# Kernel tuning notes

Measured on AMD Instinct MI355X. Metric: run time of the kernel, lower is better.

The kernel has to match this reference:

```python
import jax, jax.numpy as jnp
import numpy as np

B, L, LIP = 1, 2048, 64
HID, H, D = 3072, 24, 128
MLP = 4 * HID
CTX = 4096
EPS = 1e-6


def setup_inputs() -> dict:
    key = jax.random.key(0)
    ks = jax.random.split(key, 10)
    rn = lambda k, shape, s=1.0: jax.random.normal(k, shape, jnp.float32) * s
    x = rn(ks[0], (B, L, HID))
    vec = rn(ks[1], (B, HID))
    image_proj = rn(ks[2], (B, LIP, CTX))
    # Flux-style RoPE table: [1, 1, L, D//2, 2, 2] rotation matrices
    pos = jnp.arange(L, dtype=jnp.float32)[:, None]
    inv_freq = 1.0 / (10000.0 ** (jnp.arange(0, D, 2, dtype=jnp.float32) / D))
    ang = pos * inv_freq[None, :]                      # [L, D//2]
    cos, sin = jnp.cos(ang), jnp.sin(ang)
    pe = jnp.stack([jnp.stack([cos, -sin], -1), jnp.stack([sin, cos], -1)], -2)
    pe = pe[None, None].astype(jnp.float32)            # [1,1,L,D//2,2,2]
    return dict(
        x=x, vec=vec, pe=pe, image_proj=image_proj, ip_scale=jnp.float32(1.0),
        mod_lin_w=rn(ks[3], (3 * HID, HID), 0.02), mod_lin_b=jnp.zeros((3 * HID,), jnp.float32),
        linear1_w=rn(ks[4], (3 * HID + MLP, HID), 0.02), linear1_b=jnp.zeros((3 * HID + MLP,), jnp.float32),
        linear2_w=rn(ks[5], (HID, HID + MLP), 0.02), linear2_b=jnp.zeros((HID,), jnp.float32),
        q_norm_scale=jnp.ones((D,), jnp.float32), k_norm_scale=jnp.ones((D,), jnp.float32),
        ip_k_w=rn(ks[6], (HID, CTX), 0.02), ip_v_w=rn(ks[7], (HID, CTX), 0.02),
    )


def _layernorm(x):
    mu = jnp.mean(x, -1, keepdims=True)
    var = jnp.mean(jnp.square(x - mu), -1, keepdims=True)
    return (x - mu) * jax.lax.rsqrt(var + EPS)


def _rmsnorm(x, scale):
    return x * jax.lax.rsqrt(jnp.mean(jnp.square(x), -1, keepdims=True) + EPS) * scale


def _apply_rope(xq, pe):
    b, h, l, d = xq.shape
    xq_ = xq.reshape(b, h, l, d // 2, 1, 2)
    out = pe[..., 0] * xq_[..., 0] + pe[..., 1] * xq_[..., 1]  # [b,h,l,d//2,2]
    return out.reshape(b, h, l, d)


def _sdpa(q, k, v):
    scale = 1.0 / np.sqrt(q.shape[-1])
    s = jnp.einsum('bhqd,bhkd->bhqk', q, k) * scale
    return jnp.einsum('bhqk,bhkd->bhqd', jax.nn.softmax(s, axis=-1), v)


def _forward(x, vec, pe, image_proj, ip_scale, mod_lin_w, mod_lin_b,
             linear1_w, linear1_b, linear2_w, linear2_b,
             q_norm_scale, k_norm_scale, ip_k_w, ip_v_w):
    # modulation: shift, scale, gate from silu(vec)
    mod = jax.nn.silu(vec) @ mod_lin_w.T + mod_lin_b   # [B, 3*HID]
    shift, scale, gate = [m[:, None, :] for m in jnp.split(mod, 3, axis=-1)]
    x_mod = (1.0 + scale) * _layernorm(x) + shift
    h = x_mod @ linear1_w.T + linear1_b                # [B, L, 3*HID + MLP]
    qkv, mlp = h[..., :3 * HID], h[..., 3 * HID:]
    qkv = qkv.reshape(B, L, 3, H, D).transpose(2, 0, 3, 1, 4)  # [3,B,H,L,D]
    q, k, v = qkv[0], qkv[1], qkv[2]
    q = _rmsnorm(q, q_norm_scale)
    k = _rmsnorm(k, k_norm_scale)
    # main attention with RoPE
    attn1 = _sdpa(_apply_rope(q, pe), _apply_rope(k, pe), v)   # [B,H,L,D]
    attn1 = attn1.transpose(0, 2, 1, 3).reshape(B, L, HID)
    # IP-adapter cross-attention (query = q after QK-norm, no RoPE)
    ip_k = (image_proj @ ip_k_w.T).reshape(B, LIP, H, D).transpose(0, 2, 1, 3)
    ip_v = (image_proj @ ip_v_w.T).reshape(B, LIP, H, D).transpose(0, 2, 1, 3)
    ip_attn = _sdpa(q, ip_k, ip_v).transpose(0, 2, 1, 3).reshape(B, L, HID)
    attn_out = attn1 + ip_scale * ip_attn
    fused = jnp.concatenate([attn_out, jax.nn.gelu(mlp, approximate=True)], axis=-1)
    output = fused @ linear2_w.T + linear2_b
    return x + gate * output


def reference(x, vec, pe, image_proj, ip_scale, mod_lin_w, mod_lin_b,
              linear1_w, linear1_b, linear2_w, linear2_b,
              q_norm_scale, k_norm_scale, ip_k_w, ip_v_w):
    return _forward(x, vec, pe, image_proj, ip_scale, mod_lin_w, mod_lin_b,
                    linear1_w, linear1_b, linear2_w, linear2_b,
                    q_norm_scale, k_norm_scale, ip_k_w, ip_v_w)
```

## Files before the change

### kernel.cpp

```cpp
#include <hip/hip_runtime.h>
#include <hip/hip_bf16.h>
#include <math.h>

typedef __bf16 bf16_t;
typedef __bf16 bf16x8 __attribute__((ext_vector_type(8)));
typedef __bf16 bf16x4 __attribute__((ext_vector_type(4)));
typedef __bf16 bf16x2 __attribute__((ext_vector_type(2)));
typedef float  f32x4  __attribute__((ext_vector_type(4)));

#define HIDN 3072
#define LQ   2048
#define NH   24
#define HD   128
#define N1   21504
#define N2   15360
#define KIP  4096

__device__ __forceinline__ f32x4 mfma16(bf16x8 a, bf16x8 b, f32x4 c) {
    return __builtin_amdgcn_mfma_f32_16x16x32_bf16(a, b, c, 0, 0, 0);
}

__device__ __forceinline__ float wave_sum64(float v) {
#pragma unroll
    for (int off = 1; off < 64; off <<= 1) v += __shfl_xor(v, off);
    return v;
}

__global__ void k_convert(const float* __restrict__ in, bf16_t* __restrict__ out, int n4) {
    int i = blockIdx.x * blockDim.x + threadIdx.x;
    if (i < n4) {
        float4 f = ((const float4*)in)[i];
        bf16x4 h = {(bf16_t)f.x, (bf16_t)f.y, (bf16_t)f.z, (bf16_t)f.w};
        *(bf16x4*)(out + (size_t)i * 4) = h;
    }
}

__global__ __launch_bounds__(256) void k_mod_gemv(const float* __restrict__ vec,
                                                  const float* __restrict__ W,
                                                  const float* __restrict__ b,
                                                  float* __restrict__ mod) {
    int row  = blockIdx.x * 4 + (threadIdx.x >> 6);
    int lane = threadIdx.x & 63;
    const float4* W4 = (const float4*)(W + (size_t)row * HIDN);
    const float4* V4 = (const float4*)vec;
    float s = 0.f;
#pragma unroll
    for (int i = 0; i < 12; i++) {
        float4 w = W4[lane + i * 64];
        float4 v = V4[lane + i * 64];
        s += w.x * (v.x / (1.f + __expf(-v.x)));
        s += w.y * (v.y / (1.f + __expf(-v.y)));
        s += w.z * (v.z / (1.f + __expf(-v.z)));
        s += w.w * (v.w / (1.f + __expf(-v.w)));
    }
    s = wave_sum64(s);
    if (lane == 0) mod[row] = s + b[row];
}

__global__ __launch_bounds__(256) void k_ln_mod(const float* __restrict__ x,
                                                const float* __restrict__ mod,
                                                bf16_t* __restrict__ x_mod) {
    int row = blockIdx.x, tid = threadIdx.x;
    const float* xr = x + (size_t)row * HIDN;
    float v[12];
    float s = 0.f, ss = 0.f;
#pragma unroll
    for (int p = 0; p < 12; p++) {
        v[p] = xr[tid + p * 256];
        s += v[p]; ss += v[p] * v[p];
    }
    s = wave_sum64(s); ss = wave_sum64(ss);
    __shared__ float red[8];
    int wave = tid >> 6, lane = tid & 63;
    if (lane == 0) { red[wave] = s; red[4 + wave] = ss; }
    __syncthreads();
    float S  = red[0] + red[1] + red[2] + red[3];
    float SS = red[4] + red[5] + red[6] + red[7];
    float mean = S * (1.f / HIDN);
    float var  = SS * (1.f / HIDN) - mean * mean;
    float rstd = rsqrtf(var + 1e-6f);
#pragma unroll
    for (int p = 0; p < 12; p++) {
        int j = tid + p * 256;
        float xm = (v[p] - mean) * rstd;
        float y  = (1.f + mod[HIDN + j]) * xm + mod[j];
        x_mod[(size_t)row * HIDN + j] = (bf16_t)y;
    }
}

__device__ __forceinline__ void gemm_core(const bf16_t* __restrict__ A,
                                          const float* __restrict__ W,
                                          int K, int m0, int n0,
                                          bf16_t* a_sh, bf16_t* b_sh,
                                          f32x4 acc[4][4]) {
    const int tid = threadIdx.x;
    const int wave = tid >> 6, lane = tid & 63;
    const int qd = lane >> 4, tr = lane & 15;
    const int wm = (wave >> 1) * 64, wn = (wave & 1) * 64;
    for (int k0 = 0; k0 < K; k0 += 32) {
        __syncthreads();
#pragma unroll
        for (int i = 0; i < 2; i++) {
            int flat = tid + i * 256;
            int r = flat >> 2, s = flat & 3;
            *(bf16x8*)(a_sh + r * 40 + s * 8) =
                *(const bf16x8*)(A + (size_t)(m0 + r) * K + k0 + s * 8);
        }
#pragma unroll
        for (int i = 0; i < 4; i++) {
            int flat = tid + i * 256;
            int r = flat >> 3, s = flat & 7;
            float4 f = *(const float4*)(W + (size_t)(n0 + r) * K + k0 + s * 4);
            bf16x4 h = {(bf16_t)f.x, (bf16_t)f.y, (bf16_t)f.z, (bf16_t)f.w};
            *(bf16x4*)(b_sh + r * 40 + s * 4) = h;
        }
        __syncthreads();
        bf16x8 af[4], bfr[4];
#pragma unroll
        for (int t = 0; t < 4; t++)
            af[t] = *(const bf16x8*)(a_sh + (wm + t * 16 + tr) * 40 + qd * 8);
#pragma unroll
        for (int t = 0; t < 4; t++)
            bfr[t] = *(const bf16x8*)(b_sh + (wn + t * 16 + tr) * 40 + qd * 8);
#pragma unroll
        for (int mt = 0; mt < 4; mt++)
#pragma unroll
            for (int nt = 0; nt < 4; nt++)
                acc[mt][nt] = mfma16(af[mt], bfr[nt], acc[mt][nt]);
    }
}

__global__ __launch_bounds__(256) void k_gemm_l1(const bf16_t* __restrict__ A,
                                                 const float* __restrict__ W,
                                                 const float* __restrict__ bias,
                                                 bf16_t* __restrict__ hq,
                                                 bf16_t* __restrict__ fused) {
    __shared__ bf16_t a_sh[128 * 40];
    __shared__ bf16_t b_sh[128 * 40];
    f32x4 acc[4][4];
    const f32x4 z = {0.f, 0.f, 0.f, 0.f};
#pragma unroll
    for (int mt = 0; mt < 4; mt++)
#pragma unroll
        for (int nt = 0; nt < 4; nt++) acc[mt][nt] = z;
    int m0 = blockIdx.x * 128, n0 = blockIdx.y * 128;
    gemm_core(A, W, HIDN, m0, n0, a_sh, b_sh, acc);
    const int tid = threadIdx.x, wave = tid >> 6, lane = tid & 63;
    const int qd = lane >> 4, tr = lane & 15;
    const int wm = (wave >> 1) * 64, wn = (wave & 1) * 64;
#pragma unroll
    for (int mt = 0; mt < 4; mt++)
#pragma unroll
        for (int nt = 0; nt < 4; nt++) {
            int col = n0 + wn + nt * 16 + tr;
            float bb = bias[col];
            f32x4 v = acc[mt][nt];
#pragma unroll
            for (int r = 0; r < 4; r++) {
                int row = m0 + wm + mt * 16 + qd * 4 + r;
                float val = v[r] + bb;
                if (col < 9216) {
                    hq[(size_t)row * 9216 + col] = (bf16_t)val;
                } else {
                    float g = 0.5f * val *
                        (1.f + tanhf(0.7978845608028654f * (val + 0.044715f * val * val * val)));
                    fused[(size_t)row * N2 + HIDN + (col - 9216)] = (bf16_t)g;
                }
            }
        }
}

__global__ __launch_bounds__(256) void k_gemm_l2(const bf16_t* __restrict__ A,
                                                 const float* __restrict__ W,
                                                 const float* __restrict__ bias,
                                                 const float* __restrict__ x,
                                                 const float* __restrict__ gate,
                                                 float* __restrict__ out) {
    __shared__ bf16_t a_sh[128 * 40];
    __shared__ bf16_t b_sh[128 * 40];
    f32x4 acc[4][4];
    const f32x4 z = {0.f, 0.f, 0.f, 0.f};
#pragma unroll
    for (int mt = 0; mt < 4; mt++)
#pragma unroll
        for (int nt = 0; nt < 4; nt++) acc[mt][nt] = z;
    int m0 = blockIdx.x * 128, n0 = blockIdx.y * 128;
    gemm_core(A, W, N2, m0, n0, a_sh, b_sh, acc);
    const int tid = threadIdx.x, wave = tid >> 6, lane = tid & 63;
    const int qd = lane >> 4, tr = lane & 15;
    const int wm = (wave >> 1) * 64, wn = (wave & 1) * 64;
#pragma unroll
    for (int mt = 0; mt < 4; mt++)
#pragma unroll
        for (int nt = 0; nt < 4; nt++) {
            int col = n0 + wn + nt * 16 + tr;
            float bb = bias[col];
            float g  = gate[col];
#pragma unroll
            for (int r = 0; r < 4; r++) {
                int row = m0 + wm + mt * 16 + qd * 4 + r;
                size_t idx = (size_t)row * HIDN + col;
                out[idx] = x[idx] + g * (acc[mt][nt][r] + bb);
            }
        }
}

__global__ __launch_bounds__(256) void k_gemm_ip(const bf16_t* __restrict__ A,
                                                 const float* __restrict__ Wk,
                                                 const float* __restrict__ Wv,
                                                 bf16_t* __restrict__ outk,
                                                 bf16_t* __restrict__ outv) {
    __shared__ bf16_t a_sh[64 * 40];
    __shared__ bf16_t b_sh[64 * 40];
    const float* W = (blockIdx.y == 0) ? Wk : Wv;
    bf16_t* out    = (blockIdx.y == 0) ? outk : outv;
    int n0 = blockIdx.x * 64;
    const int tid = threadIdx.x, wave = tid >> 6, lane = tid & 63;
    const int qd = lane >> 4, tr = lane & 15;
    f32x4 acc[4];
    const f32x4 z = {0.f, 0.f, 0.f, 0.f};
#pragma unroll
    for (int mt = 0; mt < 4; mt++) acc[mt] = z;
    for (int k0 = 0; k0 < KIP; k0 += 32) {
        __syncthreads();
        {
            int r = tid >> 2, s = tid & 3;
            *(bf16x8*)(a_sh + r * 40 + s * 8) =
                *(const bf16x8*)(A + (size_t)r * KIP + k0 + s * 8);
        }
#pragma unroll
        for (int i = 0; i < 2; i++) {
            int flat = tid + i * 256;
            int r = flat >> 3, s = flat & 7;
            float4 f = *(const float4*)(W + (size_t)(n0 + r) * KIP + k0 + s * 4);
            bf16x4 h = {(bf16_t)f.x, (bf16_t)f.y, (bf16_t)f.z, (bf16_t)f.w};
            *(bf16x4*)(b_sh + r * 40 + s * 4) = h;
        }
        __syncthreads();
        bf16x8 bfrag = *(const bf16x8*)(b_sh + (wave * 16 + tr) * 40 + qd * 8);
#pragma unroll
        for (int mt = 0; mt < 4; mt++) {
            bf16x8 afrag = *(const bf16x8*)(a_sh + (mt * 16 + tr) * 40 + qd * 8);
            acc[mt] = mfma16(afrag, bfrag, acc[mt]);
        }
    }
    int col = n0 + wave * 16 + tr;
    int h = col >> 7, d = col & 127;
#pragma unroll
    for (int mt = 0; mt < 4; mt++)
#pragma unroll
        for (int r = 0; r < 4; r++) {
            int row = mt * 16 + qd * 4 + r;
            out[((size_t)h * 64 + row) * HD + d] = (bf16_t)acc[mt][r];
        }
}

__global__ __launch_bounds__(256) void k_qkv_post(const bf16_t* __restrict__ hq,
                                                  const float* __restrict__ pe,
                                                  const float* __restrict__ qs,
                                                  const float* __restrict__ ksc,
                                                  bf16_t* __restrict__ q_rope,
                                                  bf16_t* __restrict__ k_rope,
                                                  bf16_t* __restrict__ q_plain,
                                                  bf16_t* __restrict__ v_buf) {
    int wid  = blockIdx.x * 4 + (threadIdx.x >> 6);
    int lane = threadIdx.x & 63;
    int l = wid / NH, h = wid % NH;
    const bf16_t* base = hq + (size_t)l * 9216 + h * HD;
    int d0 = lane * 2;
    float q0 = (float)base[d0],        q1 = (float)base[d0 + 1];
    float k0 = (float)base[3072 + d0], k1 = (float)base[3072 + d0 + 1];
    bf16_t v0 = base[6144 + d0],       v1 = base[6144 + d0 + 1];
    float ssq = wave_sum64(q0 * q0 + q1 * q1);
    float ssk = wave_sum64(k0 * k0 + k1 * k1);
    float rq = rsqrtf(ssq * (1.f / HD) + 1e-6f);
    float rk = rsqrtf(ssk * (1.f / HD) + 1e-6f);
    float qn0 = q0 * rq * qs[d0], qn1 = q1 * rq * qs[d0 + 1];
    float kn0 = k0 * rk * ksc[d0], kn1 = k1 * rk * ksc[d0 + 1];
    const float* pp = pe + ((size_t)l * 64 + lane) * 4;
    float c00 = pp[0], c01 = pp[1], c10 = pp[2], c11 = pp[3];
    size_t oidx = ((size_t)h * LQ + l) * HD + d0;
    q_rope[oidx]     = (bf16_t)(c00 * qn0 + c01 * qn1);
    q_rope[oidx + 1] = (bf16_t)(c10 * qn0 + c11 * qn1);
    k_rope[oidx]     = (bf16_t)(c00 * kn0 + c01 * kn1);
    k_rope[oidx + 1] = (bf16_t)(c10 * kn0 + c11 * kn1);
    q_plain[oidx]     = (bf16_t)qn0;
    q_plain[oidx + 1] = (bf16_t)qn1;
    v_buf[oidx]     = v0;
    v_buf[oidx + 1] = v1;
}

__global__ __launch_bounds__(256) void k_attn(const bf16_t* __restrict__ Q,
                                              const bf16_t* __restrict__ Kb,
                                              const bf16_t* __restrict__ Vb,
                                              int Lk,
                                              bf16_t* __restrict__ out,
                                              int out_sl, int out_sh,
                                              const bf16_t* __restrict__ addsrc,
                                              const float* __restrict__ ip_scale_p) {
    __shared__ bf16_t k_sh[64 * 136];
    __shared__ bf16_t vT_sh[128 * 72];
    __shared__ bf16_t p_sh[4][16 * 72];
    const int tid = threadIdx.x, wave = tid >> 6, lane = tid & 63;
    const int qd = lane >> 4, tr = lane & 15;
    const int h = blockIdx.y;
    const int q0 = blockIdx.x * 64 + wave * 16;
    const bf16_t* Qh = Q + ((size_t)h * LQ + q0 + tr) * HD;
    bf16x8 qf[4];
#pragma unroll
    for (int ks = 0; ks < 4; ks++) qf[ks] = *(const bf16x8*)(Qh + ks * 32 + qd * 8);
    float m_r[4], l_r[4];
    f32x4 accO[8];
    const f32x4 z = {0.f, 0.f, 0.f, 0.f};
#pragma unroll
    for (int r = 0; r < 4; r++) { m_r[r] = -1e30f; l_r[r] = 0.f; }
#pragma unroll
    for (int dt = 0; dt < 8; dt++) accO[dt] = z;
    const float sc = 0.08838834764831843f;

    for (int kt = 0; kt < Lk; kt += 64) {
        __syncthreads();
        {
            int r = tid >> 2, ds = (tid & 3) * 32;
            const bf16_t* src = Kb + ((size_t)h * Lk + kt + r) * HD + ds;
#pragma unroll
            for (int u = 0; u < 4; u++)
                *(bf16x8*)(k_sh + r * 136 + ds + u * 8) = *(const bf16x8*)(src + u * 8);
        }
        {
            int kv = (tid >> 3) * 2, dv = (tid & 7) * 16;
            const bf16_t* s0 = Vb + ((size_t)h * Lk + kt + kv) * HD + dv;
            bf16x8 va0 = *(const bf16x8*)(s0);
            bf16x8 va1 = *(const bf16x8*)(s0 + 8);
            bf16x8 vb0 = *(const bf16x8*)(s0 + HD);
            bf16x8 vb1 = *(const bf16x8*)(s0 + HD + 8);
#pragma unroll
            for (int j = 0; j < 8; j++) {
                bf16x2 pr = {va0[j], vb0[j]};
                *(bf16x2*)(vT_sh + (dv + j) * 72 + kv) = pr;
            }
#pragma unroll
            for (int j = 0; j < 8; j++) {
                bf16x2 pr = {va1[j], vb1[j]};
                *(bf16x2*)(vT_sh + (dv + 8 + j) * 72 + kv) = pr;
            }
        }
        __syncthreads();
        f32x4 s4[4];
#pragma unroll
        for (int nt = 0; nt < 4; nt++) {
            f32x4 a = z;
#pragma unroll
            for (int ks = 0; ks < 4; ks++) {
                bf16x8 kf = *(const bf16x8*)(k_sh + (nt * 16 + tr) * 136 + ks * 32 + qd * 8);
                a = mfma16(qf[ks], kf, a);
            }
            s4[nt] = a;
        }
#pragma unroll
        for (int r = 0; r < 4; r++) {
            float x0 = s4[0][r] * sc, x1 = s4[1][r] * sc;
            float x2 = s4[2][r] * sc, x3 = s4[3][r] * sc;
            float mx = fmaxf(fmaxf(x0, x1), fmaxf(x2, x3));
            mx = fmaxf(mx, __shfl_xor(mx, 1));
            mx = fmaxf(mx, __shfl_xor(mx, 2));
            mx = fmaxf(mx, __shfl_xor(mx, 4));
            mx = fmaxf(mx, __shfl_xor(mx, 8));
            float mnew  = fmaxf(m_r[r], mx);
            float alpha = __expf(m_r[r] - mnew);
            m_r[r] = mnew;
            float p0 = __expf(x0 - mnew), p1 = __expf(x1 - mnew);
            float p2 = __expf(x2 - mnew), p3 = __expf(x3 - mnew);
            float rs = p0 + p1 + p2 + p3;
            rs += __shfl_xor(rs, 1);
            rs += __shfl_xor(rs, 2);
            rs += __shfl_xor(rs, 4);
            rs += __shfl_xor(rs, 8);
            l_r[r] = l_r[r] * alpha + rs;
            int prow = qd * 4 + r;
            bf16_t* pp = &p_sh[wave][prow * 72 + tr];
            pp[0]  = (bf16_t)p0;
            pp[16] = (bf16_t)p1;
            pp[32] = (bf16_t)p2;
            pp[48] = (bf16_t)p3;
#pragma unroll
            for (int dt = 0; dt < 8; dt++) accO[dt][r] *= alpha;
        }
#pragma unroll
        for (int ks2 = 0; ks2 < 2; ks2++) {
            bf16x8 pf = *(const bf16x8*)(&p_sh[wave][tr * 72 + ks2 * 32 + qd * 8]);
#pragma unroll
            for (int dt = 0; dt < 8; dt++) {
                bf16x8 vf = *(const bf16x8*)(vT_sh + (dt * 16 + tr) * 72 + ks2 * 32 + qd * 8);
                accO[dt] = mfma16(pf, vf, accO[dt]);
            }
        }
    }
    float scl = (ip_scale_p != nullptr) ? *ip_scale_p : 0.f;
#pragma unroll
    for (int dt = 0; dt < 8; dt++) {
        int d = dt * 16 + tr;
#pragma unroll
        for (int r = 0; r < 4; r++) {
            int row = q0 + qd * 4 + r;
            float o = accO[dt][r] / l_r[r];
            if (addsrc) o += scl * (float)addsrc[((size_t)h * LQ + row) * HD + d];
            out[(size_t)row * out_sl + (size_t)h * out_sh + d] = (bf16_t)o;
        }
    }
}

extern "C" void kernel_launch(void* const* d_in, const int* in_sizes, int n_in,
                              void* d_out, int out_size, void* d_ws, size_t ws_size,
                              hipStream_t stream) {
    const float* x       = (const float*)d_in[0];
    const float* vec     = (const float*)d_in[1];
    const float* pe      = (const float*)d_in[2];
    const float* ip      = (const float*)d_in[3];
    const float* ipscale = (const float*)d_in[4];
    const float* mod_w   = (const float*)d_in[5];
    const float* mod_b   = (const float*)d_in[6];
    const float* w1      = (const float*)d_in[7];
    const float* b1      = (const float*)d_in[8];
    const float* w2      = (const float*)d_in[9];
    const float* b2      = (const float*)d_in[10];
    const float* qs      = (const float*)d_in[11];
    const float* ksc     = (const float*)d_in[12];
    const float* wk      = (const float*)d_in[13];
    const float* wv      = (const float*)d_in[14];
    float* out = (float*)d_out;

    char* ws = (char*)d_ws;
    const size_t OFF_MOD   = 0;
    const size_t OFF_XMOD  = 36864;
    const size_t OFF_HQ    = OFF_XMOD + 12582912ULL;
    const size_t OFF_FUSED = OFF_HQ   + 37748736ULL;
    const size_t OFF_QR    = OFF_FUSED + 62914560ULL;
    const size_t OFF_KR    = OFF_QR + 12582912ULL;
    const size_t OFF_V     = OFF_KR + 12582912ULL;
    const size_t OFF_QP    = OFF_V  + 12582912ULL;
    const size_t OFF_IPO   = OFF_QP + 12582912ULL;
    const size_t OFF_IPB   = OFF_IPO + 12582912ULL;
    const size_t OFF_IPK   = OFF_IPB + 524288ULL;
    const size_t OFF_IPV   = OFF_IPK + 393216ULL;

    float*  mod     = (float*)(ws + OFF_MOD);
    bf16_t* x_mod   = (bf16_t*)(ws + OFF_XMOD);
    bf16_t* hq      = (bf16_t*)(ws + OFF_HQ);
    bf16_t* fused   = (bf16_t*)(ws + OFF_FUSED);
    bf16_t* q_rope  = (bf16_t*)(ws + OFF_QR);
    bf16_t* k_rope  = (bf16_t*)(ws + OFF_KR);
    bf16_t* v_buf   = (bf16_t*)(ws + OFF_V);
    bf16_t* q_plain = (bf16_t*)(ws + OFF_QP);
    bf16_t* ip_out  = (bf16_t*)(ws + OFF_IPO);
    bf16_t* ipb     = (bf16_t*)(ws + OFF_IPB);
    bf16_t* ipk     = (bf16_t*)(ws + OFF_IPK);
    bf16_t* ipv     = (bf16_t*)(ws + OFF_IPV);

    k_convert<<<256, 256, 0, stream>>>(ip, ipb, 65536);
    k_mod_gemv<<<2304, 256, 0, stream>>>(vec, mod_w, mod_b, mod);
    k_ln_mod<<<2048, 256, 0, stream>>>(x, mod, x_mod);
    k_gemm_l1<<<dim3(16, 168), 256, 0, stream>>>(x_mod, w1, b1, hq, fused);
    k_qkv_post<<<12288, 256, 0, stream>>>(hq, pe, qs, ksc, q_rope, k_rope, q_plain, v_buf);
    k_gemm_ip<<<dim3(48, 2), 256, 0, stream>>>(ipb, wk, wv, ipk, ipv);
    k_attn<<<dim3(32, 24), 256, 0, stream>>>(q_plain, ipk, ipv, 64,
                                             ip_out, HD, LQ * HD, nullptr, nullptr);
    k_attn<<<dim3(32, 24), 256, 0, stream>>>(q_rope, k_rope, v_buf, LQ,
                                             fused, N2, HD, ip_out, ipscale);
    k_gemm_l2<<<dim3(16, 24), 256, 0, stream>>>(fused, w2, b2, x, mod + 6144, out);
}
```

Baseline: 1.897 ms.

## Pre-convert weights to bf16 and load GEMM tiles via global_load_lds

When the workspace is large enough, the fp32 weight matrices are converted to bf16 in a separate pass before each GEMM, and the GEMM cores then stream A and W tiles straight into LDS with the direct global-to-LDS load builtin. The goal is to stop each tile block from re-reading fp32 weights and converting them on every k-step, which halves per-tile weight bandwidth and removes register staging. The cost is extra conversion kernels that read and write every weight once per call. LDS rows are now unpadded (stride 32), which may add bank conflicts on the fragment reads, and the old fp32 path is kept as a fallback.

```diff
diff --git a/kernel.cpp b/kernel.cpp
--- a/kernel.cpp
+++ b/kernel.cpp
@@ -24,6 +24,12 @@
 #pragma unroll
     for (int off = 1; off < 64; off <<= 1) v += __shfl_xor(v, off);
     return v;
+}
+
+__device__ __forceinline__ void gld16(bf16_t* dst_lds, const bf16_t* src) {
+    __builtin_amdgcn_global_load_lds(
+        (const __attribute__((address_space(1))) void*)src,
+        (__attribute__((address_space(3))) void*)dst_lds, 16, 0, 0);
 }
 
 __global__ void k_convert(const float* __restrict__ in, bf16_t* __restrict__ out, int n4) {
@@ -88,40 +94,36 @@
     }
 }
 
-__device__ __forceinline__ void gemm_core(const bf16_t* __restrict__ A,
-                                          const float* __restrict__ W,
-                                          int K, int m0, int n0,
-                                          bf16_t* a_sh, bf16_t* b_sh,
-                                          f32x4 acc[4][4]) {
+__device__ __forceinline__ void gemm_core_b(const bf16_t* __restrict__ A,
+                                            const bf16_t* __restrict__ W,
+                                            int K, int m0, int n0,
+                                            bf16_t* a_sh, bf16_t* b_sh,
+                                            f32x4 acc[4][4]) {
     const int tid = threadIdx.x;
     const int wave = tid >> 6, lane = tid & 63;
     const int qd = lane >> 4, tr = lane & 15;
     const int wm = (wave >> 1) * 64, wn = (wave & 1) * 64;
+    const int r = tid >> 2, s = tid & 3;
+    const bf16_t* Ab  = A + (size_t)(m0 + r) * K + s * 8;
+    const bf16_t* Ab2 = Ab + (size_t)64 * K;
+    const bf16_t* Wb  = W + (size_t)(n0 + r) * K + s * 8;
+    const bf16_t* Wb2 = Wb + (size_t)64 * K;
+    bf16_t* a_dst = a_sh + wave * 512;
+    bf16_t* b_dst = b_sh + wave * 512;
     for (int k0 = 0; k0 < K; k0 += 32) {
         __syncthreads();
-#pragma unroll
-        for (int i = 0; i < 2; i++) {
-            int flat = tid + i * 256;
-            int r = flat >> 2, s = flat & 3;
-            *(bf16x8*)(a_sh + r * 40 + s * 8) =
-                *(const bf16x8*)(A + (size_t)(m0 + r) * K + k0 + s * 8);
-        }
-#pragma unroll
-        for (int i = 0; i < 4; i++) {
-            int flat = tid + i * 256;
-            int r = flat >> 3, s = flat & 7;
-            float4 f = *(const float4*)(W + (size_t)(n0 + r) * K + k0 + s * 4);
-            bf16x4 h = {(bf16_t)f.x, (bf16_t)f.y, (bf16_t)f.z, (bf16_t)f.w};
-            *(bf16x4*)(b_sh + r * 40 + s * 4) = h;
-        }
+        gld16(a_dst,        Ab  + k0);
+        gld16(a_dst + 2048, Ab2 + k0);
+        gld16(b_dst,        Wb  + k0);
+        gld16(b_dst + 2048, Wb2 + k0);
         __syncthreads();
         bf16x8 af[4], bfr[4];
 #pragma unroll
         for (int t = 0; t < 4; t++)
-            af[t] = *(const bf16x8*)(a_sh + (wm + t * 16 + tr) * 40 + qd * 8);
+            af[t] = *(const bf16x8*)(a_sh + (wm + t * 16 + tr) * 32 + qd * 8);
 #pragma unroll
         for (int t = 0; t < 4; t++)
-            bfr[t] = *(const bf16x8*)(b_sh + (wn + t * 16 + tr) * 40 + qd * 8);
+            bfr[t] = *(const bf16x8*)(b_sh + (wn + t * 16 + tr) * 32 + qd * 8);
 #pragma unroll
         for (int mt = 0; mt < 4; mt++)
 #pragma unroll
@@ -130,13 +132,13 @@
     }
 }
 
-__global__ __launch_bounds__(256) void k_gemm_l1(const bf16_t* __restrict__ A,
-                                                 const float* __restrict__ W,
-                                                 const float* __restrict__ bias,
-                                                 bf16_t* __restrict__ hq,
-                                                 bf16_t* __restrict__ fused) {
-    __shared__ bf16_t a_sh[128 * 40];
-    __shared__ bf16_t b_sh[128 * 40];
+__global__ __launch_bounds__(256) void k_gemm_l1_b(const bf16_t* __restrict__ A,
+                                                   const bf16_t* __restrict__ W,
+                                                   const float* __restrict__ bias,
+                                                   bf16_t* __restrict__ hq,
+                                                   bf16_t* __restrict__ fused) {
+    __shared__ bf16_t a_sh[128 * 32];
+    __shared__ bf16_t b_sh[128 * 32];
     f32x4 acc[4][4];
     const f32x4 z = {0.f, 0.f, 0.f, 0.f};
 #pragma unroll
@@ -144,7 +146,7 @@
 #pragma unroll
         for (int nt = 0; nt < 4; nt++) acc[mt][nt] = z;
     int m0 = blockIdx.x * 128, n0 = blockIdx.y * 128;
-    gemm_core(A, W, HIDN, m0, n0, a_sh, b_sh, acc);
+    gemm_core_b(A, W, HIDN, m0, n0, a_sh, b_sh, acc);
     const int tid = threadIdx.x, wave = tid >> 6, lane = tid & 63;
     const int qd = lane >> 4, tr = lane & 15;
     const int wm = (wave >> 1) * 64, wn = (wave & 1) * 64;
@@ -170,12 +172,132 @@
         }
 }
 
-__global__ __launch_bounds__(256) void k_gemm_l2(const bf16_t* __restrict__ A,
-                                                 const float* __restrict__ W,
-                                                 const float* __restrict__ bias,
-                                                 const float* __restrict__ x,
-                                                 const float* __restrict__ gate,
-                                                 float* __restrict__ out) {
+__global__ __launch_bounds__(256) void k_gemm_l2_b(const bf16_t* __restrict__ A,
+                                                   const bf16_t* __restrict__ W,
+                                                   const float* __restrict__ bias,
+                                                   const float* __restrict__ x,
+                                                   const float* __restrict__ gate,
+                                                   float* __restrict__ out) {
+    __shared__ bf16_t a_sh[128 * 32];
+    __shared__ bf16_t b_sh[128 * 32];
+    f32x4 acc[4][4];
+    const f32x4 z = {0.f, 0.f, 0.f, 0.f};
+#pragma unroll
+    for (int mt = 0; mt < 4; mt++)
+#pragma unroll
+        for (int nt = 0; nt < 4; nt++) acc[mt][nt] = z;
+    int m0 = blockIdx.x * 128, n0 = blockIdx.y * 128;
+    gemm_core_b(A, W, N2, m0, n0, a_sh, b_sh, acc);
+    const int tid = threadIdx.x, wave = tid >> 6, lane = tid & 63;
+    const int qd = lane >> 4, tr = lane & 15;
+    const int wm = (wave >> 1) * 64, wn = (wave & 1) * 64;
+#pragma unroll
+    for (int mt = 0; mt < 4; mt++)
+#pragma unroll
+        for (int nt = 0; nt < 4; nt++) {
+            int col = n0 + wn + nt * 16 + tr;
+            float bb = bias[col];
+            float g  = gate[col];
+#pragma unroll
+            for (int r = 0; r < 4; r++) {
+                int row = m0 + wm + mt * 16 + qd * 4 + r;
+                size_t idx = (size_t)row * HIDN + col;
+                out[idx] = x[idx] + g * (acc[mt][nt][r] + bb);
+            }
+        }
+}
+
+__global__ __launch_bounds__(256) void k_gemm_ip_b(const bf16_t* __restrict__ A,
+                                                   const bf16_t* __restrict__ Wk,
+                                                   const bf16_t* __restrict__ Wv,
+                                                   bf16_t* __restrict__ outk,
+                                                   bf16_t* __restrict__ outv) {
+    __shared__ bf16_t a_sh[64 * 32];
+    __shared__ bf16_t b_sh[64 * 32];
+    const bf16_t* W = (blockIdx.y == 0) ? Wk : Wv;
+    bf16_t* out    = (blockIdx.y == 0) ? outk : outv;
+    int n0 = blockIdx.x * 64;
+    const int tid = threadIdx.x, wave = tid >> 6, lane = tid & 63;
+    const int qd = lane >> 4, tr = lane & 15;
+    const int r = tid >> 2, s = tid & 3;
+    const bf16_t* Ab = A + (size_t)r * KIP + s * 8;
+    const bf16_t* Wb = W + (size_t)(n0 + r) * KIP + s * 8;
+    bf16_t* a_dst = a_sh + wave * 512;
+    bf16_t* b_dst = b_sh + wave * 512;
+    f32x4 acc[4];
+    const f32x4 z = {0.f, 0.f, 0.f, 0.f};
+#pragma unroll
+    for (int mt = 0; mt < 4; mt++) acc[mt] = z;
+    for (int k0 = 0; k0 < KIP; k0 += 32) {
+        __syncthreads();
+        gld16(a_dst, Ab + k0);
+        gld16(b_dst, Wb + k0);
+        __syncthreads();
+        bf16x8 bfrag = *(const bf16x8*)(b_sh + (wave * 16 + tr) * 32 + qd * 8);
+#pragma unroll
+        for (int mt = 0; mt < 4; mt++) {
+            bf16x8 afrag = *(const bf16x8*)(a_sh + (mt * 16 + tr) * 32 + qd * 8);
+            acc[mt] = mfma16(afrag, bfrag, acc[mt]);
+        }
+    }
+    int col = n0 + wave * 16 + tr;
+    int h = col >> 7, d = col & 127;
+#pragma unroll
+    for (int mt = 0; mt < 4; mt++)
+#pragma unroll
+        for (int r2 = 0; r2 < 4; r2++) {
+            int row = mt * 16 + qd * 4 + r2;
+            out[((size_t)h * 64 + row) * HD + d] = (bf16_t)acc[mt][r2];
+        }
+}
+
+__device__ __forceinline__ void gemm_core_f32(const bf16_t* __restrict__ A,
+                                              const float* __restrict__ W,
+                                              int K, int m0, int n0,
+                                              bf16_t* a_sh, bf16_t* b_sh,
+                                              f32x4 acc[4][4]) {
+    const int tid = threadIdx.x;
+    const int wave = tid >> 6, lane = tid & 63;
+    const int qd = lane >> 4, tr = lane & 15;
+    const int wm = (wave >> 1) * 64, wn = (wave & 1) * 64;
+    for (int k0 = 0; k0 < K; k0 += 32) {
+        __syncthreads();
+#pragma unroll
+        for (int i = 0; i < 2; i++) {
+            int flat = tid + i * 256;
+            int r = flat >> 2, s = flat & 3;
+            *(bf16x8*)(a_sh + r * 40 + s * 8) =
+                *(const bf16x8*)(A + (size_t)(m0 + r) * K + k0 + s * 8);
+        }
+#pragma unroll
+        for (int i = 0; i < 4; i++) {
+            int flat = tid + i * 256;
+            int r = flat >> 3, s = flat & 7;
+            float4 f = *(const float4*)(W + (size_t)(n0 + r) * K + k0 + s * 4);
+            bf16x4 h = {(bf16_t)f.x, (bf16_t)f.y, (bf16_t)f.z, (bf16_t)f.w};
+            *(bf16x4*)(b_sh + r * 40 + s * 4) = h;
+        }
+        __syncthreads();
+        bf16x8 af[4], bfr[4];
+#pragma unroll
+        for (int t = 0; t < 4; t++)
+            af[t] = *(const bf16x8*)(a_sh + (wm + t * 16 + tr) * 40 + qd * 8);
+#pragma unroll
+        for (int t = 0; t < 4; t++)
+            bfr[t] = *(const bf16x8*)(b_sh + (wn + t * 16 + tr) * 40 + qd * 8);
+#pragma unroll
+        for (int mt = 0; mt < 4; mt++)
+#pragma unroll
+            for (int nt = 0; nt < 4; nt++)
+                acc[mt][nt] = mfma16(af[mt], bfr[nt], acc[mt][nt]);
+    }
+}
+
+__global__ __launch_bounds__(256) void k_gemm_l1_f(const bf16_t* __restrict__ A,
+                                                   const float* __restrict__ W,
+                                                   const float* __restrict__ bias,
+                                                   bf16_t* __restrict__ hq,
+                                                   bf16_t* __restrict__ fused) {
     __shared__ bf16_t a_sh[128 * 40];
     __shared__ bf16_t b_sh[128 * 40];
     f32x4 acc[4][4];
@@ -185,7 +307,48 @@
 #pragma unroll
         for (int nt = 0; nt < 4; nt++) acc[mt][nt] = z;
     int m0 = blockIdx.x * 128, n0 = blockIdx.y * 128;
-    gemm_core(A, W, N2, m0, n0, a_sh, b_sh, acc);
+    gemm_core_f32(A, W, HIDN, m0, n0, a_sh, b_sh, acc);
+    const int tid = threadIdx.x, wave = tid >> 6, lane = tid & 63;
+    const int qd = lane >> 4, tr = lane & 15;
+    const int wm = (wave >> 1) * 64, wn = (wave & 1) * 64;
+#pragma unroll
+    for (int mt = 0; mt < 4; mt++)
+#pragma unroll
+        for (int nt = 0; nt < 4; nt++) {
+            int col = n0 + wn + nt * 16 + tr;
+            float bb = bias[col];
+            f32x4 v = acc[mt][nt];
+#pragma unroll
+            for (int r = 0; r < 4; r++) {
+                int row = m0 + wm + mt * 16 + qd * 4 + r;
+                float val = v[r] + bb;
+                if (col < 9216) {
+                    hq[(size_t)row * 9216 + col] = (bf16_t)val;
+                } else {
+                    float g = 0.5f * val *
+                        (1.f + tanhf(0.7978845608028654f * (val + 0.044715f * val * val * val)));
+                    fused[(size_t)row * N2 + HIDN + (col - 9216)] = (bf16_t)g;
+                }
+            }
+        }
+}
+
+__global__ __launch_bounds__(256) void k_gemm_l2_f(const bf16_t* __restrict__ A,
+                                                   const float* __restrict__ W,
+                                                   const float* __restrict__ bias,
+                                                   const float* __restrict__ x,
+                                                   const float* __restrict__ gate,
+                                                   float* __restrict__ out) {
+    __shared__ bf16_t a_sh[128 * 40];
+    __shared__ bf16_t b_sh[128 * 40];
+    f32x4 acc[4][4];
+    const f32x4 z = {0.f, 0.f, 0.f, 0.f};
+#pragma unroll
+    for (int mt = 0; mt < 4; mt++)
+#pragma unroll
+        for (int nt = 0; nt < 4; nt++) acc[mt][nt] = z;
+    int m0 = blockIdx.x * 128, n0 = blockIdx.y * 128;
+    gemm_core_f32(A, W, N2, m0, n0, a_sh, b_sh, acc);
     const int tid = threadIdx.x, wave = tid >> 6, lane = tid & 63;
     const int qd = lane >> 4, tr = lane & 15;
     const int wm = (wave >> 1) * 64, wn = (wave & 1) * 64;
@@ -205,11 +368,11 @@
         }
 }
 
-__global__ __launch_bounds__(256) void k_gemm_ip(const bf16_t* __restrict__ A,
-                                                 const float* __restrict__ Wk,
-                                                 const float* __restrict__ Wv,
-                                                 bf16_t* __restrict__ outk,
-                                                 bf16_t* __restrict__ outv) {
+__global__ __launch_bounds__(256) void k_gemm_ip_f(const bf16_t* __restrict__ A,
+                                                   const float* __restrict__ Wk,
+                                                   const float* __restrict__ Wv,
+                                                   bf16_t* __restrict__ outk,
+                                                   bf16_t* __restrict__ outv) {
     __shared__ bf16_t a_sh[64 * 40];
     __shared__ bf16_t b_sh[64 * 40];
     const float* W = (blockIdx.y == 0) ? Wk : Wv;
@@ -443,6 +606,9 @@
     const size_t OFF_IPB   = OFF_IPO + 12582912ULL;
     const size_t OFF_IPK   = OFF_IPB + 524288ULL;
     const size_t OFF_IPV   = OFF_IPK + 393216ULL;
+    const size_t OFF_WB    = OFF_IPV + 393216ULL;
+    const size_t WB_BYTES  = 132120576ULL;
+    const size_t WS_NEED   = OFF_WB + WB_BYTES;
 
     float*  mod     = (float*)(ws + OFF_MOD);
     bf16_t* x_mod   = (bf16_t*)(ws + OFF_XMOD);
@@ -456,16 +622,42 @@
     bf16_t* ipb     = (bf16_t*)(ws + OFF_IPB);
     bf16_t* ipk     = (bf16_t*)(ws + OFF_IPK);
     bf16_t* ipv     = (bf16_t*)(ws + OFF_IPV);
+    bf16_t* wbuf    = (bf16_t*)(ws + OFF_WB);
+
+    const bool big_ws = (ws_size >= WS_NEED);
 
     k_convert<<<256, 256, 0, stream>>>(ip, ipb, 65536);
     k_mod_gemv<<<2304, 256, 0, stream>>>(vec, mod_w, mod_b, mod);
     k_ln_mod<<<2048, 256, 0, stream>>>(x, mod, x_mod);
-    k_gemm_l1<<<dim3(16, 168), 256, 0, stream>>>(x_mod, w1, b1, hq, fused);
+
+    if (big_ws) {
+        k_convert<<<64512, 256, 0, stream>>>(w1, wbuf, 16515072);
+        k_gemm_l1_b<<<dim3(16, 168), 256, 0, stream>>>(x_mod, wbuf, b1, hq, fused);
+    } else {
+        k_gemm_l1_f<<<dim3(16, 168), 256, 0, stream>>>(x_mod, w1, b1, hq, fused);
+    }
+
     k_qkv_post<<<12288, 256, 0, stream>>>(hq, pe, qs, ksc, q_rope, k_rope, q_plain, v_buf);
-    k_gemm_ip<<<dim3(48, 2), 256, 0, stream>>>(ipb, wk, wv, ipk, ipv);
+
+    if (big_ws) {
+        bf16_t* wkb = wbuf;
+        bf16_t* wvb = wbuf + 12582912;
+        k_convert<<<12288, 256, 0, stream>>>(wk, wkb, 3145728);
+        k_convert<<<12288, 256, 0, stream>>>(wv, wvb, 3145728);
+        k_gemm_ip_b<<<dim3(48, 2), 256, 0, stream>>>(ipb, wkb, wvb, ipk, ipv);
+    } else {
+        k_gemm_ip_f<<<dim3(48, 2), 256, 0, stream>>>(ipb, wk, wv, ipk, ipv);
+    }
+
     k_attn<<<dim3(32, 24), 256, 0, stream>>>(q_plain, ipk, ipv, 64,
                                              ip_out, HD, LQ * HD, nullptr, nullptr);
     k_attn<<<dim3(32, 24), 256, 0, stream>>>(q_rope, k_rope, v_buf, LQ,
                                              fused, N2, HD, ip_out, ipscale);
-    k_gemm_l2<<<dim3(16, 24), 256, 0, stream>>>(fused, w2, b2, x, mod + 6144, out);
-}
+
+    if (big_ws) {
+        k_convert<<<46080, 256, 0, stream>>>(w2, wbuf, 11796480);
+        k_gemm_l2_b<<<dim3(16, 24), 256, 0, stream>>>(fused, wbuf, b2, x, mod + 6144, out);
+    } else {
+        k_gemm_l2_f<<<dim3(16, 24), 256, 0, stream>>>(fused, w2, b2, x, mod + 6144, out);
+    }
+}
```

After: 1.624 ms. 1.17x faster.
